# Optimization experiments

Measured on AMD Instinct MI355X. Metric: run time of the kernel, lower is better.

Reference implementation:

```python
import jax, jax.numpy as jnp
import numpy as np

N, M, P = 8192, 8192, 16


def setup_inputs() -> dict:
    key = jax.random.key(0)
    k1, k2, k3, k4, k5 = jax.random.split(key, 5)
    x1 = jax.random.normal(k1, (N, P), dtype=jnp.float32)
    x2 = jax.random.normal(k2, (M, P), dtype=jnp.float32)
    # flax initializers.uniform() draws in [0, 0.01); use small scalars
    log_sigma_b = jax.random.uniform(k3, (), dtype=jnp.float32) * 0.01
    log_sigma_v = jax.random.uniform(k4, (), dtype=jnp.float32) * 0.01
    offset = jax.random.uniform(k5, (), dtype=jnp.float32) * 0.01
    return {"x1": x1, "x2": x2, "log_sigma_b": log_sigma_b,
            "log_sigma_v": log_sigma_v, "offset": offset}


def reference(x1, x2, log_sigma_b, log_sigma_v, offset):
    sigma_b = jnp.exp(log_sigma_b)
    sigma_v = jnp.exp(log_sigma_v)
    # sum_p (x1-offset)(x2-offset) as a dot product (n,p)@(p,m) -> (n,m)
    d = jnp.einsum("np,mp->nm", x1 - offset, x2 - offset)
    K = sigma_v ** 2 * d + sigma_b ** 2
    return K
```

## Files before the change

### kernel.cpp

```cpp
#include <hip/hip_runtime.h>
#include <cmath>


typedef float f32x4 __attribute__((ext_vector_type(4)));

#define TILE 64
#define LDST 68

__global__ __launch_bounds__(256, 8) void linear_kernel(
    const float* __restrict__ x1, const float* __restrict__ x2,
    const float* __restrict__ p_lsb, const float* __restrict__ p_lsv,
    const float* __restrict__ p_off, float* __restrict__ out, int m)
{
    __shared__ float s1[16 * LDST];
    __shared__ float s2[16 * LDST];

    const int tid = threadIdx.x;
    const int tx  = tid & 15;
    const int ty  = tid >> 4;
    const int n0  = blockIdx.y * TILE;
    const int m0  = blockIdx.x * TILE;

    const float off = p_off[0];
    const float sv  = expf(p_lsv[0]);
    const float sb  = expf(p_lsb[0]);
    const float sb2 = sb * sb;

    {
        const int row = tid >> 2;
        const int q   = tid & 3;
        const f32x4 v = ((const f32x4*)(x1 + (size_t)(n0 + row) * 16))[q];
        const f32x4 w = ((const f32x4*)(x2 + (size_t)(m0 + row) * 16))[q];
        #pragma unroll
        for (int j = 0; j < 4; ++j) {
            s1[(q * 4 + j) * LDST + row] = sv * (v[j] - off);
            s2[(q * 4 + j) * LDST + row] = sv * (w[j] - off);
        }
    }

    float acc[4][4];
    #pragma unroll
    for (int r = 0; r < 4; ++r)
        #pragma unroll
        for (int c = 0; c < 4; ++c) acc[r][c] = 0.0f;

    __syncthreads();

    #pragma unroll
    for (int p = 0; p < 16; ++p) {
        const f32x4 a4 = *(const f32x4*)&s1[p * LDST + ty * 4];
        const f32x4 b4 = *(const f32x4*)&s2[p * LDST + tx * 4];
        #pragma unroll
        for (int r = 0; r < 4; ++r)
            #pragma unroll
            for (int c = 0; c < 4; ++c)
                acc[r][c] = fmaf(a4[r], b4[c], acc[r][c]);
    }

    float* orow = out + (size_t)(n0 + ty * 4) * m + m0 + tx * 4;
    #pragma unroll
    for (int r = 0; r < 4; ++r) {
        f32x4 o;
        o[0] = acc[r][0] + sb2;
        o[1] = acc[r][1] + sb2;
        o[2] = acc[r][2] + sb2;
        o[3] = acc[r][3] + sb2;
        *(f32x4*)orow = o;
        orow += m;
    }
}

extern "C" void kernel_launch(void* const* d_in, const int* in_sizes, int n_in,
                              void* d_out, int out_size, void* d_ws, size_t ws_size,
                              hipStream_t stream) {
    const float* x1  = (const float*)d_in[0];
    const float* x2  = (const float*)d_in[1];
    const float* lsb = (const float*)d_in[2];
    const float* lsv = (const float*)d_in[3];
    const float* off = (const float*)d_in[4];
    float* out = (float*)d_out;

    const int n = in_sizes[0] / 16;
    const int m = in_sizes[1] / 16;

    dim3 grid(m / TILE, n / TILE);
    linear_kernel<<<grid, 256, 0, stream>>>(x1, x2, lsb, lsv, off, out, m);
}
```

Measured before the change: 335.5 us.

## Use 128x128 tiles with 8x8 per-thread outputs and double-buffered x2 tiles

Each block now computes a 128-row strip across four consecutive 128-column tiles. Each thread holds an 8x8 accumulator, and the next x2 tile is prefetched into a double-buffered LDS region while the current tile is computed and stored. The aim is to amortise the x1 load and per-block setup over more output and to raise FMA work per LDS read. In exchange it uses more registers (launch bounds drop to 4 blocks per CU) and launches fewer blocks. The kernel is output-write bound (256 MB written), so the benefit may be small.

```diff
diff --git a/kernel.cpp b/kernel.cpp
--- a/kernel.cpp
+++ b/kernel.cpp
@@ -4,22 +4,23 @@
 
 typedef float f32x4 __attribute__((ext_vector_type(4)));
 
-#define TILE 64
-#define LDST 68
+#define TILE   128
+#define LDST   132
+#define MTILES 4
 
-__global__ __launch_bounds__(256, 8) void linear_kernel(
+__global__ __launch_bounds__(256, 4) void linear_kernel(
     const float* __restrict__ x1, const float* __restrict__ x2,
     const float* __restrict__ p_lsb, const float* __restrict__ p_lsv,
     const float* __restrict__ p_off, float* __restrict__ out, int m)
 {
     __shared__ float s1[16 * LDST];
-    __shared__ float s2[16 * LDST];
+    __shared__ float s2[2][16 * LDST];
 
     const int tid = threadIdx.x;
     const int tx  = tid & 15;
     const int ty  = tid >> 4;
     const int n0  = blockIdx.y * TILE;
-    const int m0  = blockIdx.x * TILE;
+    const int mg  = blockIdx.x * MTILES;
 
     const float off = p_off[0];
     const float sv  = expf(p_lsv[0]);
@@ -27,46 +28,93 @@
     const float sb2 = sb * sb;
 
     {
-        const int row = tid >> 2;
-        const int q   = tid & 3;
-        const f32x4 v = ((const f32x4*)(x1 + (size_t)(n0 + row) * 16))[q];
-        const f32x4 w = ((const f32x4*)(x2 + (size_t)(m0 + row) * 16))[q];
+        const f32x4* g1 = (const f32x4*)(x1 + (size_t)n0 * 16);
+        const f32x4* g2 = (const f32x4*)(x2 + (size_t)(mg * TILE) * 16);
         #pragma unroll
-        for (int j = 0; j < 4; ++j) {
-            s1[(q * 4 + j) * LDST + row] = sv * (v[j] - off);
-            s2[(q * 4 + j) * LDST + row] = sv * (w[j] - off);
+        for (int j = tid; j < 512; j += 256) {
+            const int row = j >> 2;
+            const int p0  = (j & 3) * 4;
+            const f32x4 v = g1[j];
+            const f32x4 w = g2[j];
+            #pragma unroll
+            for (int jj = 0; jj < 4; ++jj) {
+                s1[(p0 + jj) * LDST + row]    = sv * (v[jj] - off);
+                s2[0][(p0 + jj) * LDST + row] = sv * (w[jj] - off);
+            }
         }
     }
+    asm volatile("s_waitcnt lgkmcnt(0)" ::: "memory");
+    __builtin_amdgcn_s_barrier();
+    __builtin_amdgcn_sched_barrier(0);
 
-    float acc[4][4];
+    int cur = 0;
     #pragma unroll
-    for (int r = 0; r < 4; ++r)
+    for (int mt = 0; mt < MTILES; ++mt) {
+        f32x4 pf0, pf1;
+        if (mt < MTILES - 1) {
+            const f32x4* gn =
+                (const f32x4*)(x2 + (size_t)((mg + mt + 1) * TILE) * 16);
+            pf0 = gn[tid];
+            pf1 = gn[tid + 256];
+        }
+
+        float acc[8][8];
         #pragma unroll
-        for (int c = 0; c < 4; ++c) acc[r][c] = 0.0f;
+        for (int r = 0; r < 8; ++r)
+            #pragma unroll
+            for (int c = 0; c < 8; ++c) acc[r][c] = 0.0f;
 
-    __syncthreads();
+        const float* s2c = s2[cur];
+        #pragma unroll
+        for (int p = 0; p < 16; ++p) {
+            const float* s1p = &s1[p * LDST];
+            const float* s2p = &s2c[p * LDST];
+            const f32x4 a0 = *(const f32x4*)&s1p[ty * 4];
+            const f32x4 a1 = *(const f32x4*)&s1p[64 + ty * 4];
+            const f32x4 b0 = *(const f32x4*)&s2p[tx * 4];
+            const f32x4 b1 = *(const f32x4*)&s2p[64 + tx * 4];
+            const float av[8] = {a0[0], a0[1], a0[2], a0[3],
+                                 a1[0], a1[1], a1[2], a1[3]};
+            const float bv[8] = {b0[0], b0[1], b0[2], b0[3],
+                                 b1[0], b1[1], b1[2], b1[3]};
+            #pragma unroll
+            for (int r = 0; r < 8; ++r)
+                #pragma unroll
+                for (int c = 0; c < 8; ++c)
+                    acc[r][c] = fmaf(av[r], bv[c], acc[r][c]);
+        }
 
-    #pragma unroll
-    for (int p = 0; p < 16; ++p) {
-        const f32x4 a4 = *(const f32x4*)&s1[p * LDST + ty * 4];
-        const f32x4 b4 = *(const f32x4*)&s2[p * LDST + tx * 4];
-        #pragma unroll
-        for (int r = 0; r < 4; ++r)
+        {
+            const int m0 = (mg + mt) * TILE;
             #pragma unroll
-            for (int c = 0; c < 4; ++c)
-                acc[r][c] = fmaf(a4[r], b4[c], acc[r][c]);
-    }
+            for (int r = 0; r < 8; ++r) {
+                const int lr = (r < 4) ? (ty * 4 + r) : (64 + ty * 4 + (r - 4));
+                float* orow = out + (size_t)(n0 + lr) * m + m0;
+                f32x4 o0, o1;
+                #pragma unroll
+                for (int c = 0; c < 4; ++c) {
+                    o0[c] = acc[r][c] + sb2;
+                    o1[c] = acc[r][4 + c] + sb2;
+                }
+                *(f32x4*)&orow[tx * 4]      = o0;
+                *(f32x4*)&orow[64 + tx * 4] = o1;
+            }
+        }
 
-    float* orow = out + (size_t)(n0 + ty * 4) * m + m0 + tx * 4;
-    #pragma unroll
-    for (int r = 0; r < 4; ++r) {
-        f32x4 o;
-        o[0] = acc[r][0] + sb2;
-        o[1] = acc[r][1] + sb2;
-        o[2] = acc[r][2] + sb2;
-        o[3] = acc[r][3] + sb2;
-        *(f32x4*)orow = o;
-        orow += m;
+        if (mt < MTILES - 1) {
+            float* s2n = s2[cur ^ 1];
+            const int row = tid >> 2;
+            const int p0  = (tid & 3) * 4;
+            #pragma unroll
+            for (int jj = 0; jj < 4; ++jj) {
+                s2n[(p0 + jj) * LDST + row]      = sv * (pf0[jj] - off);
+                s2n[(p0 + jj) * LDST + row + 64] = sv * (pf1[jj] - off);
+            }
+            asm volatile("s_waitcnt lgkmcnt(0)" ::: "memory");
+            __builtin_amdgcn_s_barrier();
+            __builtin_amdgcn_sched_barrier(0);
+            cur ^= 1;
+        }
     }
 }
 
@@ -83,6 +131,6 @@
     const int n = in_sizes[0] / 16;
     const int m = in_sizes[1] / 16;
 
-    dim3 grid(m / TILE, n / TILE);
+    dim3 grid(m / (TILE * MTILES), n / TILE);
     linear_kernel<<<grid, 256, 0, stream>>>(x1, x2, lsb, lsv, off, out, m);
 }
```

Measured after the change: 419.3 us. 25.0% more time.
